# Optimization experiments

Measured on AMD Instinct MI355X. Metric: run time of the kernel, lower is better.

The kernel has to match this reference:

```python
import jax, jax.numpy as jnp
import numpy as np

W_L1, W_NORMAL, W_LAPLACIAN = 1.0, 1.0, 0.1
NORM_EPS = 1e-6   # F.normalize eps
COS_EPS = 1e-8    # F.cosine_similarity default eps


def setup_inputs() -> dict:
    key = jax.random.key(0)
    k1, k2, k3, k4, k5, k6 = jax.random.split(key, 6)
    N, F, NNZ = 1_000_000, 2_000_000, 8_000_000
    return {
        "V_rec": jax.random.normal(k1, (N, 3), dtype=jnp.float32),
        "V_gt": jax.random.normal(k2, (N, 3), dtype=jnp.float32),
        "faces": jax.random.randint(k3, (F, 3), 0, N, dtype=jnp.int64)
        if jax.config.jax_enable_x64 else jax.random.randint(k3, (F, 3), 0, N, dtype=jnp.int32),
        "L_rows": jax.random.randint(k4, (NNZ,), 0, N, dtype=jnp.int32),
        "L_cols": jax.random.randint(k5, (NNZ,), 0, N, dtype=jnp.int32),
        "L_vals": jax.random.normal(k6, (NNZ,), dtype=jnp.float32),
    }


def _vertex_normals(verts, faces):
    # gather verts by face indices: [F,3] each
    v0 = verts[faces[:, 0]]
    v1 = verts[faces[:, 1]]
    v2 = verts[faces[:, 2]]
    face_normals = jnp.cross(v1 - v0, v2 - v0)  # [F,3]
    vn = (jnp.zeros_like(verts)
          .at[faces[:, 0]].add(face_normals)
          .at[faces[:, 1]].add(face_normals)
          .at[faces[:, 2]].add(face_normals))
    norm = jnp.linalg.norm(vn, axis=1, keepdims=True)
    return vn / jnp.maximum(norm, NORM_EPS)


def _cosine_sim(a, b):
    dot = jnp.sum(a * b, axis=1)
    na = jnp.linalg.norm(a, axis=1)
    nb = jnp.linalg.norm(b, axis=1)
    return dot / (jnp.maximum(na, COS_EPS) * jnp.maximum(nb, COS_EPS))


def _spmm(rows, cols, vals, V):
    # sparse [N,N] @ dense [N,3] via gather + segment_sum
    return jax.ops.segment_sum(vals[:, None] * V[cols], rows, num_segments=V.shape[0])


def reference(V_rec, V_gt, faces, L_rows, L_cols, L_vals):
    # L1 term
    loss_l1 = jnp.mean(jnp.abs(V_rec - V_gt))
    # Normal cosine term
    normals_gt = _vertex_normals(V_gt, faces)
    normals_rec = _vertex_normals(V_rec, faces)
    cos_n = jnp.nan_to_num(_cosine_sim(normals_rec, normals_gt), nan=1.0)
    loss_normal = jnp.mean(1.0 - cos_n)
    # Laplacian cosine term
    delta_gt = _spmm(L_rows, L_cols, L_vals, V_gt)
    delta_rec = _spmm(L_rows, L_cols, L_vals, V_rec)
    cos_l = jnp.nan_to_num(_cosine_sim(delta_rec, delta_gt), nan=1.0)
    loss_laplacian = jnp.mean(1.0 - cos_l)
    finite = jnp.isfinite(delta_gt).all() & jnp.isfinite(delta_rec).all()
    loss_laplacian = jnp.where(finite, loss_laplacian, 0.0)
    return W_L1 * loss_l1 + W_NORMAL * loss_normal + W_LAPLACIAN * loss_laplacian
```

## Files before the change

### kernel.cpp

```cpp
#include <hip/hip_runtime.h>
#include <hip/hip_bf16.h>

#define NORM_EPS_F 1e-6f
#define COS_EPS_F  1e-8f
#define BK   512
#define BKSH 9
#define NBGMAX 2048
#define CHF1 2048
#define CHL1 4096
#define K2   32

__device__ __forceinline__ void atomAddF(float* p, float v) {
    unsafeAtomicAdd(p, v);
}

template<int NV>
__device__ __forceinline__ void blockReduceAtomicN(float (&v)[NV], float* dst) {
    #pragma unroll
    for (int off = 32; off > 0; off >>= 1) {
        #pragma unroll
        for (int k = 0; k < NV; ++k) v[k] += __shfl_down(v[k], off, 64);
    }
    __shared__ float red[4][NV];
    int wave = threadIdx.x >> 6, lane = threadIdx.x & 63;
    if (lane == 0) {
        #pragma unroll
        for (int k = 0; k < NV; ++k) red[wave][k] = v[k];
    }
    __syncthreads();
    if (threadIdx.x == 0) {
        float s[NV];
        #pragma unroll
        for (int k = 0; k < NV; ++k) s[k] = 0.f;
        for (int w = 0; w < 4; ++w)
            #pragma unroll
            for (int k = 0; k < NV; ++k) s[k] += red[w][k];
        #pragma unroll
        for (int k = 0; k < NV; ++k) atomAddF(&dst[k], s[k]);
    }
}


__global__ void __launch_bounds__(256) pack_l1_kernel(
    const float* __restrict__ Vr, const float* __restrict__ Vg,
    float4* __restrict__ Vp, float* __restrict__ accum, int N)
{
    int i = blockIdx.x * blockDim.x + threadIdx.x;
    float l1[1] = {0.f};
    if (i < N) {
        float rx = Vr[3 * i], ry = Vr[3 * i + 1], rz = Vr[3 * i + 2];
        float gx = Vg[3 * i], gy = Vg[3 * i + 1], gz = Vg[3 * i + 2];
        Vp[2 * i]     = make_float4(rx, ry, rz, 0.f);
        Vp[2 * i + 1] = make_float4(gx, gy, gz, 0.f);
        l1[0] = fabsf(rx - gx) + fabsf(ry - gy) + fabsf(rz - gz);
    }
    blockReduceAtomicN<1>(l1, &accum[0]);
}

__global__ void __launch_bounds__(256) fn_kernel(
    const float4* __restrict__ Vp, const int* __restrict__ faces,
    float4* __restrict__ FN, int F)
{
    int half = (F + 1) >> 1;
    int t = blockIdx.x * blockDim.x + threadIdx.x;
    if (t >= half) return;
    int fi[2] = {t, t + half};
    int n = (fi[1] < F) ? 2 : 1;
    int idx[2][3];
    #pragma unroll
    for (int k = 0; k < 2; ++k) if (k < n) {
        idx[k][0] = faces[3 * fi[k]];
        idx[k][1] = faces[3 * fi[k] + 1];
        idx[k][2] = faces[3 * fi[k] + 2];
    }
    float4 r0[2], r1[2], r2[2], g0[2], g1[2], g2[2];
    #pragma unroll
    for (int k = 0; k < 2; ++k) if (k < n) {
        r0[k] = Vp[2 * idx[k][0]]; g0[k] = Vp[2 * idx[k][0] + 1];
        r1[k] = Vp[2 * idx[k][1]]; g1[k] = Vp[2 * idx[k][1] + 1];
        r2[k] = Vp[2 * idx[k][2]]; g2[k] = Vp[2 * idx[k][2] + 1];
    }
    #pragma unroll
    for (int k = 0; k < 2; ++k) if (k < n) {
        float ax = r1[k].x - r0[k].x, ay = r1[k].y - r0[k].y, az = r1[k].z - r0[k].z;
        float bx = r2[k].x - r0[k].x, by = r2[k].y - r0[k].y, bz = r2[k].z - r0[k].z;
        FN[2 * fi[k]] = make_float4(ay * bz - az * by, az * bx - ax * bz, ax * by - ay * bx, 0.f);
        ax = g1[k].x - g0[k].x; ay = g1[k].y - g0[k].y; az = g1[k].z - g0[k].z;
        bx = g2[k].x - g0[k].x; by = g2[k].y - g0[k].y; bz = g2[k].z - g0[k].z;
        FN[2 * fi[k] + 1] = make_float4(ay * bz - az * by, az * bx - ax * bz, ax * by - ay * bx, 0.f);
    }
}


__global__ void __launch_bounds__(256) bucket_F1(
    const int* __restrict__ faces, int* __restrict__ cntC,
    unsigned* __restrict__ recA, unsigned char* __restrict__ recC,
    int capC, int F, int b0, int bcnt, int chunk)
{
    __shared__ int hist[64];
    int f0 = blockIdx.x * chunk, f1 = min(f0 + chunk, F);
    if (threadIdx.x < 64) hist[threadIdx.x] = 0;
    __syncthreads();
    for (int f = f0 + threadIdx.x; f < f1; f += 256) {
        #pragma unroll
        for (int c = 0; c < 3; ++c) {
            unsigned fb = ((unsigned)faces[3 * f + c] >> BKSH) - (unsigned)b0;
            if (fb < (unsigned)bcnt) atomicAdd(&hist[fb >> 5], 1);
        }
    }
    __syncthreads();
    if (threadIdx.x < 64) {
        int h = hist[threadIdx.x];
        if (h) hist[threadIdx.x] = atomicAdd(&cntC[threadIdx.x], h);
    }
    __syncthreads();
    for (int f = f0 + threadIdx.x; f < f1; f += 256) {
        #pragma unroll
        for (int c = 0; c < 3; ++c) {
            int v = faces[3 * f + c];
            unsigned fb = ((unsigned)v >> BKSH) - (unsigned)b0;
            if (fb < (unsigned)bcnt) {
                int pos = atomicAdd(&hist[fb >> 5], 1);
                if (pos < capC) {
                    size_t idx = (size_t)(fb >> 5) * capC + pos;
                    recA[idx] = ((unsigned)f << BKSH) | ((unsigned)v & (BK - 1));
                    recC[idx] = (unsigned char)(fb & 31);
                }
            }
        }
    }
}

__global__ void __launch_bounds__(256) bucket_L1(
    const int* __restrict__ rows, const int* __restrict__ cols,
    const float* __restrict__ vals, int* __restrict__ cntC,
    int2* __restrict__ recA, unsigned char* __restrict__ recC,
    int capC, int nnz, int b0, int bcnt, int chunk)
{
    __shared__ int hist[64];
    int i0 = blockIdx.x * chunk, i1 = min(i0 + chunk, nnz);
    if (threadIdx.x < 64) hist[threadIdx.x] = 0;
    __syncthreads();
    for (int i = i0 + threadIdx.x; i < i1; i += 256) {
        unsigned fb = ((unsigned)rows[i] >> BKSH) - (unsigned)b0;
        if (fb < (unsigned)bcnt) atomicAdd(&hist[fb >> 5], 1);
    }
    __syncthreads();
    if (threadIdx.x < 64) {
        int h = hist[threadIdx.x];
        if (h) hist[threadIdx.x] = atomicAdd(&cntC[threadIdx.x], h);
    }
    __syncthreads();
    for (int i = i0 + threadIdx.x; i < i1; i += 256) {
        int r = rows[i];
        unsigned fb = ((unsigned)r >> BKSH) - (unsigned)b0;
        if (fb < (unsigned)bcnt) {
            int pos = atomicAdd(&hist[fb >> 5], 1);
            if (pos < capC) {
                size_t idx = (size_t)(fb >> 5) * capC + pos;
                recA[idx] = make_int2(
                    (int)(((unsigned)cols[i] << BKSH) | ((unsigned)r & (BK - 1))),
                    __float_as_int(vals[i]));
                recC[idx] = (unsigned char)(fb & 31);
            }
        }
    }
}


__global__ void __launch_bounds__(256) bucket_F2(
    const int* __restrict__ cntC, const unsigned* __restrict__ recA,
    const unsigned char* __restrict__ recC, int capC,
    int* __restrict__ cntFine, unsigned* __restrict__ fine, int capF)
{
    __shared__ int hist[32];
    int c = blockIdx.x;
    int K = gridDim.y, k = blockIdx.y;
    int ch = (capC + K - 1) / K;
    int n = min(cntC[c], capC);
    int i0 = k * ch, i1 = min(i0 + ch, n);
    if (threadIdx.x < 32) hist[threadIdx.x] = 0;
    __syncthreads();
    const size_t base = (size_t)c * capC;
    for (int i = i0 + threadIdx.x; i < i1; i += 256)
        atomicAdd(&hist[recC[base + i]], 1);
    __syncthreads();
    if (threadIdx.x < 32) {
        int h = hist[threadIdx.x];
        if (h) hist[threadIdx.x] = atomicAdd(&cntFine[(c << 5) + threadIdx.x], h);
    }
    __syncthreads();
    for (int i = i0 + threadIdx.x; i < i1; i += 256) {
        int fic = recC[base + i];
        int pos = atomicAdd(&hist[fic], 1);
        if (pos < capF)
            fine[(size_t)((c << 5) + fic) * capF + pos] = recA[base + i];
    }
}

__global__ void __launch_bounds__(256) bucket_L2(
    const int* __restrict__ cntC, const int2* __restrict__ recA,
    const unsigned char* __restrict__ recC, int capC,
    int* __restrict__ cntFine, int2* __restrict__ fine, int capL)
{
    __shared__ int hist[32];
    int c = blockIdx.x;
    int K = gridDim.y, k = blockIdx.y;
    int ch = (capC + K - 1) / K;
    int n = min(cntC[c], capC);
    int i0 = k * ch, i1 = min(i0 + ch, n);
    if (threadIdx.x < 32) hist[threadIdx.x] = 0;
    __syncthreads();
    const size_t base = (size_t)c * capC;
    for (int i = i0 + threadIdx.x; i < i1; i += 256)
        atomicAdd(&hist[recC[base + i]], 1);
    __syncthreads();
    if (threadIdx.x < 32) {
        int h = hist[threadIdx.x];
        if (h) hist[threadIdx.x] = atomicAdd(&cntFine[(c << 5) + threadIdx.x], h);
    }
    __syncthreads();
    for (int i = i0 + threadIdx.x; i < i1; i += 256) {
        int fic = recC[base + i];
        int pos = atomicAdd(&hist[fic], 1);
        if (pos < capL)
            fine[(size_t)((c << 5) + fic) * capL + pos] = recA[base + i];
    }
}


__global__ void __launch_bounds__(256) accum_normals_kernel(
    const float4* __restrict__ Vp, const float4* __restrict__ FN,
    const int* __restrict__ faces,
    const int* __restrict__ cnt, const unsigned* __restrict__ recF, int capF,
    float* __restrict__ accum, int N, int b0, int use_fn)
{
    __shared__ float vnr[3 * BK];
    __shared__ float vng[3 * BK];
    int g = blockIdx.x;
    for (int i = threadIdx.x; i < 3 * BK; i += blockDim.x) { vnr[i] = 0.f; vng[i] = 0.f; }
    __syncthreads();

    const unsigned* rec = recF + (size_t)g * capF;
    int n = min(cnt[g], capF);
    int i = threadIdx.x;
    if (use_fn) {
        for (; i + 768 < n; i += 1024) {
            unsigned rc[4];
            rc[0] = rec[i]; rc[1] = rec[i + 256]; rc[2] = rec[i + 512]; rc[3] = rec[i + 768];
            float4 nr[4], ng[4];
            #pragma unroll
            for (int k = 0; k < 4; ++k) {
                int f = rc[k] >> BKSH;
                nr[k] = FN[2 * f];
                ng[k] = FN[2 * f + 1];
            }
            #pragma unroll
            for (int k = 0; k < 4; ++k) {
                int lv = rc[k] & (BK - 1);
                atomicAdd(&vnr[3 * lv + 0], nr[k].x);
                atomicAdd(&vnr[3 * lv + 1], nr[k].y);
                atomicAdd(&vnr[3 * lv + 2], nr[k].z);
                atomicAdd(&vng[3 * lv + 0], ng[k].x);
                atomicAdd(&vng[3 * lv + 1], ng[k].y);
                atomicAdd(&vng[3 * lv + 2], ng[k].z);
            }
        }
    }
    for (; i < n; i += 256) {
        unsigned rc = rec[i];
        int lv = rc & (BK - 1);
        int f  = rc >> BKSH;
        float4 nr, ng;
        if (use_fn) {
            nr = FN[2 * f];
            ng = FN[2 * f + 1];
        } else {
            int i0 = faces[3 * f], i1 = faces[3 * f + 1], i2 = faces[3 * f + 2];
            float4 r0 = Vp[2 * i0], r1 = Vp[2 * i1], r2 = Vp[2 * i2];
            float4 g0 = Vp[2 * i0 + 1], g1 = Vp[2 * i1 + 1], g2 = Vp[2 * i2 + 1];
            float ax = r1.x - r0.x, ay = r1.y - r0.y, az = r1.z - r0.z;
            float bx = r2.x - r0.x, by = r2.y - r0.y, bz = r2.z - r0.z;
            nr = make_float4(ay * bz - az * by, az * bx - ax * bz, ax * by - ay * bx, 0.f);
            ax = g1.x - g0.x; ay = g1.y - g0.y; az = g1.z - g0.z;
            bx = g2.x - g0.x; by = g2.y - g0.y; bz = g2.z - g0.z;
            ng = make_float4(ay * bz - az * by, az * bx - ax * bz, ax * by - ay * bx, 0.f);
        }
        atomicAdd(&vnr[3 * lv + 0], nr.x);
        atomicAdd(&vnr[3 * lv + 1], nr.y);
        atomicAdd(&vnr[3 * lv + 2], nr.z);
        atomicAdd(&vng[3 * lv + 0], ng.x);
        atomicAdd(&vng[3 * lv + 1], ng.y);
        atomicAdd(&vng[3 * lv + 2], ng.z);
    }
    __syncthreads();

    float ln[1] = {0.f};
    for (int lv = threadIdx.x; lv < BK; lv += blockDim.x) {
        int gv = ((b0 + g) << BKSH) + lv;
        if (gv < N) {
            float ax = vnr[3 * lv], ay = vnr[3 * lv + 1], az = vnr[3 * lv + 2];
            float bx = vng[3 * lv], by = vng[3 * lv + 1], bz = vng[3 * lv + 2];
            float na = sqrtf(ax * ax + ay * ay + az * az);
            float nb = sqrtf(bx * bx + by * by + bz * bz);
            float ia = 1.0f / fmaxf(na, NORM_EPS_F);
            float ib = 1.0f / fmaxf(nb, NORM_EPS_F);
            ax *= ia; ay *= ia; az *= ia;
            bx *= ib; by *= ib; bz *= ib;
            float dot = ax * bx + ay * by + az * bz;
            float nna = sqrtf(ax * ax + ay * ay + az * az);
            float nnb = sqrtf(bx * bx + by * by + bz * bz);
            float cosn = dot / (fmaxf(nna, COS_EPS_F) * fmaxf(nnb, COS_EPS_F));
            if (isnan(cosn)) cosn = 1.0f;
            ln[0] += 1.0f - cosn;
        }
    }
    blockReduceAtomicN<1>(ln, &accum[1]);
}

__global__ void __launch_bounds__(256) accum_lap_kernel(
    const float4* __restrict__ Vp,
    const int* __restrict__ cnt, const int2* __restrict__ recL, int capL,
    float* __restrict__ accum, int N, int b0)
{
    __shared__ float dlr[3 * BK];
    __shared__ float dlg[3 * BK];
    int g = blockIdx.x;
    for (int i = threadIdx.x; i < 3 * BK; i += blockDim.x) { dlr[i] = 0.f; dlg[i] = 0.f; }
    __syncthreads();

    const int2* rec = recL + (size_t)g * capL;
    int n = min(cnt[g], capL);
    int i = threadIdx.x;
    for (; i + 768 < n; i += 1024) {
        int2 rc[4];
        rc[0] = rec[i]; rc[1] = rec[i + 256]; rc[2] = rec[i + 512]; rc[3] = rec[i + 768];
        float4 pr[4], pg[4];
        #pragma unroll
        for (int k = 0; k < 4; ++k) {
            int col = (unsigned)rc[k].x >> BKSH;
            pr[k] = Vp[2 * col];
            pg[k] = Vp[2 * col + 1];
        }
        #pragma unroll
        for (int k = 0; k < 4; ++k) {
            int lv = (unsigned)rc[k].x & (BK - 1);
            float v = __int_as_float(rc[k].y);
            atomicAdd(&dlr[3 * lv + 0], v * pr[k].x);
            atomicAdd(&dlr[3 * lv + 1], v * pr[k].y);
            atomicAdd(&dlr[3 * lv + 2], v * pr[k].z);
            atomicAdd(&dlg[3 * lv + 0], v * pg[k].x);
            atomicAdd(&dlg[3 * lv + 1], v * pg[k].y);
            atomicAdd(&dlg[3 * lv + 2], v * pg[k].z);
        }
    }
    for (; i < n; i += 256) {
        int2 rc = rec[i];
        unsigned u = (unsigned)rc.x;
        int lv  = u & (BK - 1);
        int col = u >> BKSH;
        float v = __int_as_float(rc.y);
        float4 pr = Vp[2 * col];
        float4 pg = Vp[2 * col + 1];
        atomicAdd(&dlr[3 * lv + 0], v * pr.x);
        atomicAdd(&dlr[3 * lv + 1], v * pr.y);
        atomicAdd(&dlr[3 * lv + 2], v * pr.z);
        atomicAdd(&dlg[3 * lv + 0], v * pg.x);
        atomicAdd(&dlg[3 * lv + 1], v * pg.y);
        atomicAdd(&dlg[3 * lv + 2], v * pg.z);
    }
    __syncthreads();

    float vals2[2] = {0.f, 0.f};
    for (int lv = threadIdx.x; lv < BK; lv += blockDim.x) {
        int gv = ((b0 + g) << BKSH) + lv;
        if (gv < N) {
            float px = dlr[3 * lv], py = dlr[3 * lv + 1], pz = dlr[3 * lv + 2];
            float qx = dlg[3 * lv], qy = dlg[3 * lv + 1], qz = dlg[3 * lv + 2];
            bool fin = isfinite(px) && isfinite(py) && isfinite(pz) &&
                       isfinite(qx) && isfinite(qy) && isfinite(qz);
            vals2[1] += fin ? 0.f : 1.f;
            float dotl = px * qx + py * qy + pz * qz;
            float npn = sqrtf(px * px + py * py + pz * pz);
            float nqn = sqrtf(qx * qx + qy * qy + qz * qz);
            float cosl = dotl / (fmaxf(npn, COS_EPS_F) * fmaxf(nqn, COS_EPS_F));
            if (isnan(cosl)) cosl = 1.0f;
            vals2[0] += 1.0f - cosl;
        }
    }
    blockReduceAtomicN<2>(vals2, &accum[2]);
}

__global__ void finalize_kernel(const float* __restrict__ accum,
                                float* __restrict__ out, int N)
{
    float invN = 1.0f / (float)N;
    float l1 = accum[0] * invN * (1.0f / 3.0f);
    float ln = accum[1] * invN;
    float ll = (accum[3] > 0.0f) ? 0.0f : accum[2] * invN;
    out[0] = 1.0f * l1 + 1.0f * ln + 0.1f * ll;
}


__global__ void __launch_bounds__(256) face_normals_kernel(
    const float* __restrict__ Vr, const float* __restrict__ Vg,
    const int* __restrict__ faces,
    float* __restrict__ vn_rec, float* __restrict__ vn_gt, int F)
{
    int f = blockIdx.x * blockDim.x + threadIdx.x;
    if (f >= F) return;
    int i0 = faces[3 * f + 0], i1 = faces[3 * f + 1], i2 = faces[3 * f + 2];
    {
        float v0x = Vr[3 * i0], v0y = Vr[3 * i0 + 1], v0z = Vr[3 * i0 + 2];
        float v1x = Vr[3 * i1], v1y = Vr[3 * i1 + 1], v1z = Vr[3 * i1 + 2];
        float v2x = Vr[3 * i2], v2y = Vr[3 * i2 + 1], v2z = Vr[3 * i2 + 2];
        float ax = v1x - v0x, ay = v1y - v0y, az = v1z - v0z;
        float bx = v2x - v0x, by = v2y - v0y, bz = v2z - v0z;
        float nx = ay * bz - az * by, ny = az * bx - ax * bz, nz = ax * by - ay * bx;
        atomAddF(&vn_rec[3 * i0], nx); atomAddF(&vn_rec[3 * i0 + 1], ny); atomAddF(&vn_rec[3 * i0 + 2], nz);
        atomAddF(&vn_rec[3 * i1], nx); atomAddF(&vn_rec[3 * i1 + 1], ny); atomAddF(&vn_rec[3 * i1 + 2], nz);
        atomAddF(&vn_rec[3 * i2], nx); atomAddF(&vn_rec[3 * i2 + 1], ny); atomAddF(&vn_rec[3 * i2 + 2], nz);
    }
    {
        float v0x = Vg[3 * i0], v0y = Vg[3 * i0 + 1], v0z = Vg[3 * i0 + 2];
        float v1x = Vg[3 * i1], v1y = Vg[3 * i1 + 1], v1z = Vg[3 * i1 + 2];
        float v2x = Vg[3 * i2], v2y = Vg[3 * i2 + 1], v2z = Vg[3 * i2 + 2];
        float ax = v1x - v0x, ay = v1y - v0y, az = v1z - v0z;
        float bx = v2x - v0x, by = v2y - v0y, bz = v2z - v0z;
        float nx = ay * bz - az * by, ny = az * bx - ax * bz, nz = ax * by - ay * bx;
        atomAddF(&vn_gt[3 * i0], nx); atomAddF(&vn_gt[3 * i0 + 1], ny); atomAddF(&vn_gt[3 * i0 + 2], nz);
        atomAddF(&vn_gt[3 * i1], nx); atomAddF(&vn_gt[3 * i1 + 1], ny); atomAddF(&vn_gt[3 * i1 + 2], nz);
        atomAddF(&vn_gt[3 * i2], nx); atomAddF(&vn_gt[3 * i2 + 1], ny); atomAddF(&vn_gt[3 * i2 + 2], nz);
    }
}

__global__ void __launch_bounds__(256) spmm_kernel(
    const float* __restrict__ Vr, const float* __restrict__ Vg,
    const int* __restrict__ rows, const int* __restrict__ cols,
    const float* __restrict__ vals,
    float* __restrict__ dl_rec, float* __restrict__ dl_gt, int nnz)
{
    int i = blockIdx.x * blockDim.x + threadIdx.x;
    if (i >= nnz) return;
    int r = rows[i], c = cols[i];
    float v = vals[i];
    atomAddF(&dl_rec[3 * r], v * Vr[3 * c]);
    atomAddF(&dl_rec[3 * r + 1], v * Vr[3 * c + 1]);
    atomAddF(&dl_rec[3 * r + 2], v * Vr[3 * c + 2]);
    atomAddF(&dl_gt[3 * r], v * Vg[3 * c]);
    atomAddF(&dl_gt[3 * r + 1], v * Vg[3 * c + 1]);
    atomAddF(&dl_gt[3 * r + 2], v * Vg[3 * c + 2]);
}

__global__ void __launch_bounds__(256) reduce_kernel(
    const float* __restrict__ Vr, const float* __restrict__ Vg,
    const float* __restrict__ vn_rec, const float* __restrict__ vn_gt,
    const float* __restrict__ dl_rec, const float* __restrict__ dl_gt,
    float* __restrict__ accum, int N)
{
    int i = blockIdx.x * blockDim.x + threadIdx.x;
    float l1 = 0.0f, ln = 0.0f, ll = 0.0f, nonfin = 0.0f;
    if (i < N) {
        float rx = Vr[3 * i], ry = Vr[3 * i + 1], rz = Vr[3 * i + 2];
        float gx = Vg[3 * i], gy = Vg[3 * i + 1], gz = Vg[3 * i + 2];
        l1 = fabsf(rx - gx) + fabsf(ry - gy) + fabsf(rz - gz);
        float ax = vn_rec[3 * i], ay = vn_rec[3 * i + 1], az = vn_rec[3 * i + 2];
        float bx = vn_gt[3 * i],  by = vn_gt[3 * i + 1],  bz = vn_gt[3 * i + 2];
        float na = sqrtf(ax * ax + ay * ay + az * az);
        float nb = sqrtf(bx * bx + by * by + bz * bz);
        float ia = 1.0f / fmaxf(na, NORM_EPS_F);
        float ib = 1.0f / fmaxf(nb, NORM_EPS_F);
        ax *= ia; ay *= ia; az *= ia; bx *= ib; by *= ib; bz *= ib;
        float dot = ax * bx + ay * by + az * bz;
        float nna = sqrtf(ax * ax + ay * ay + az * az);
        float nnb = sqrtf(bx * bx + by * by + bz * bz);
        float cosn = dot / (fmaxf(nna, COS_EPS_F) * fmaxf(nnb, COS_EPS_F));
        if (isnan(cosn)) cosn = 1.0f;
        ln = 1.0f - cosn;
        float px = dl_rec[3 * i], py = dl_rec[3 * i + 1], pz = dl_rec[3 * i + 2];
        float qx = dl_gt[3 * i],  qy = dl_gt[3 * i + 1],  qz = dl_gt[3 * i + 2];
        bool fin = isfinite(px) && isfinite(py) && isfinite(pz) &&
                   isfinite(qx) && isfinite(qy) && isfinite(qz);
        nonfin = fin ? 0.0f : 1.0f;
        float dotl = px * qx + py * qy + pz * qz;
        float npn = sqrtf(px * px + py * py + pz * pz);
        float nqn = sqrtf(qx * qx + qy * qy + qz * qz);
        float cosl = dotl / (fmaxf(npn, COS_EPS_F) * fmaxf(nqn, COS_EPS_F));
        if (isnan(cosl)) cosl = 1.0f;
        ll = 1.0f - cosl;
    }
    float a[1] = {l1};  blockReduceAtomicN<1>(a, &accum[0]);
    float b[1] = {ln};  blockReduceAtomicN<1>(b, &accum[1]);
    float c2[2] = {ll, nonfin}; blockReduceAtomicN<2>(c2, &accum[2]);
}


extern "C" void kernel_launch(void* const* d_in, const int* in_sizes, int n_in,
                              void* d_out, int out_size, void* d_ws, size_t ws_size,
                              hipStream_t stream)
{
    const float* Vr    = (const float*)d_in[0];
    const float* Vg    = (const float*)d_in[1];
    const int*   faces = (const int*)d_in[2];
    const int*   Lr    = (const int*)d_in[3];
    const int*   Lc    = (const int*)d_in[4];
    const float* Lv    = (const float*)d_in[5];

    const int N   = in_sizes[0] / 3;
    const int F   = in_sizes[2] / 3;
    const int NNZ = in_sizes[3];
    const int NB  = (N + BK - 1) >> BKSH;

    float* ws = (float*)d_ws;
    const int B = 256;

    const long long totW   = (long long)(ws_size / 4);
    const long long fixedW = 4 + 64 + NBGMAX;
    const long long vpW    = 8LL * N;
    const long long arenaW = totW - fixedW - vpW;
    const long long fnW    = 8LL * F;

    const int capF = 3 * F / (NB > 0 ? NB : 1) + 1 + 640;
    const int capL = NNZ / (NB > 0 ? NB : 1) + 1 + 640;

    auto fwords = [&](int nbg) -> long long {
        long long nc = (nbg + 31) / 32, capC = 32LL * capF;
        return nc * capC + (nc * capC + 3) / 4 + (long long)nbg * capF + 4;
    };
    auto lwords = [&](int nbg) -> long long {
        long long nc = (nbg + 31) / 32, capC = 32LL * capL;
        return nc * capC * 2 + (((nc * capC + 3) / 4 + 1) & ~1LL) + (long long)nbg * capL * 2 + 4;
    };

    int NBG_F = NB < NBGMAX ? NB : NBGMAX;
    bool tierA = (arenaW - fnW) >= fwords(64);
    long long arenaF = tierA ? (arenaW - fnW) : arenaW;
    while (NBG_F > 64 && fwords(NBG_F) > arenaF) NBG_F -= 32;
    int NBG_L = NB < NBGMAX ? NB : NBGMAX;
    while (NBG_L > 64 && lwords(NBG_L) > arenaW) NBG_L -= 32;

    bool fast = (N <= (1 << 20)) && (F <= (1 << 22)) &&
                NBG_F >= 64 && NBG_L >= 64 &&
                fwords(NBG_F) <= arenaF && lwords(NBG_L) <= arenaW &&
                arenaW > 0;

    if (fast) {
        float*  accum   = ws;
        int*    cntC    = (int*)(ws + 4);
        int*    cntFine = (int*)(ws + 68);
        float4* Vp      = (float4*)(ws + fixedW);
        float*  arena   = ws + fixedW + vpW;

        const long long NCF = (NBG_F + 31) / 32, capCF = 32LL * capF;
        float4*        FN    = (float4*)arena;
        float*         fbase = tierA ? (arena + fnW) : arena;
        unsigned*      recAF = (unsigned*)fbase;
        unsigned char* recCF = (unsigned char*)(recAF + NCF * capCF);
        unsigned*      fineF = (unsigned*)(fbase + NCF * capCF + (NCF * capCF + 3) / 4);

        const long long NCL = (NBG_L + 31) / 32, capCL = 32LL * capL;
        int2*          recAL = (int2*)arena;
        unsigned char* recCL = (unsigned char*)(recAL + NCL * capCL);
        const long long bytesWL = ((NCL * capCL + 3) / 4 + 1) & ~1LL;
        int2*          fineL = (int2*)(arena + NCL * capCL * 2 + bytesWL);

        hipMemsetAsync(accum, 0, 4 * sizeof(float), stream);

        pack_l1_kernel<<<dim3((N + B - 1) / B), dim3(B), 0, stream>>>(Vr, Vg, Vp, accum, N);
        if (tierA) {
            int half = (F + 1) >> 1;
            fn_kernel<<<dim3((half + B - 1) / B), dim3(B), 0, stream>>>(Vp, faces, FN, F);
        }

        int passF = (NB + NBG_F - 1) / NBG_F;
        for (int p = 0; p < passF; ++p) {
            int b0 = p * NBG_F;
            int bcnt = NB - b0 < NBG_F ? NB - b0 : NBG_F;
            int nc = (bcnt + 31) / 32;
            hipMemsetAsync(ws + 4, 0, (64 + NBGMAX) * sizeof(int), stream);
            bucket_F1<<<dim3((F + CHF1 - 1) / CHF1), dim3(B), 0, stream>>>(
                faces, cntC, recAF, recCF, (int)capCF, F, b0, bcnt, CHF1);
            bucket_F2<<<dim3(nc, K2), dim3(B), 0, stream>>>(
                cntC, recAF, recCF, (int)capCF, cntFine, fineF, capF);
            accum_normals_kernel<<<dim3(bcnt), dim3(B), 0, stream>>>(
                Vp, FN, faces, cntFine, fineF, capF, accum, N, b0, tierA ? 1 : 0);
        }

        int passL = (NB + NBG_L - 1) / NBG_L;
        for (int p = 0; p < passL; ++p) {
            int b0 = p * NBG_L;
            int bcnt = NB - b0 < NBG_L ? NB - b0 : NBG_L;
            int nc = (bcnt + 31) / 32;
            hipMemsetAsync(ws + 4, 0, (64 + NBGMAX) * sizeof(int), stream);
            bucket_L1<<<dim3((NNZ + CHL1 - 1) / CHL1), dim3(B), 0, stream>>>(
                Lr, Lc, Lv, cntC, recAL, recCL, (int)capCL, NNZ, b0, bcnt, CHL1);
            bucket_L2<<<dim3(nc, K2), dim3(B), 0, stream>>>(
                cntC, recAL, recCL, (int)capCL, cntFine, fineL, capL);
            accum_lap_kernel<<<dim3(bcnt), dim3(B), 0, stream>>>(
                Vp, cntFine, fineL, capL, accum, N, b0);
        }
        finalize_kernel<<<dim3(1), dim3(1), 0, stream>>>(accum, (float*)d_out, N);
    } else {
        float* vn_rec = ws;
        float* vn_gt  = ws + (size_t)3 * N;
        float* dl_rec = ws + (size_t)6 * N;
        float* dl_gt  = ws + (size_t)9 * N;
        float* accum  = ws + (size_t)12 * N;
        hipMemsetAsync(d_ws, 0, ((size_t)12 * N + 4) * sizeof(float), stream);
        face_normals_kernel<<<dim3((F + B - 1) / B), dim3(B), 0, stream>>>(Vr, Vg, faces, vn_rec, vn_gt, F);
        spmm_kernel<<<dim3((NNZ + B - 1) / B), dim3(B), 0, stream>>>(Vr, Vg, Lr, Lc, Lv, dl_rec, dl_gt, NNZ);
        reduce_kernel<<<dim3((N + B - 1) / B), dim3(B), 0, stream>>>(Vr, Vg, vn_rec, vn_gt, dl_rec, dl_gt, accum, N);
        finalize_kernel<<<dim3(1), dim3(1), 0, stream>>>(accum, (float*)d_out, N);
    }
}
```

Baseline: 1.098 ms.

## Sub-bucket Laplacian records by column octant to localize vertex gathers

Bucket_L1 now encodes the high bits of the column index (an octant of the vertex range) into the per-record byte, and bucket_L2 splits each row bucket into 8 column-octant sub-buckets. The accumulate kernel walks the octants in order, so the vertex gathers of concurrently running blocks fall within a narrower address range and should hit cache more often. The cost is more fine-bucket counters, a larger 256-entry histogram, per-sub-bucket capacity padding that can overflow under skew, and a shallower unroll in the inner loop.

```diff
diff --git a/kernel.cpp b/kernel.cpp
--- a/kernel.cpp
+++ b/kernel.cpp
@@ -9,6 +9,7 @@
 #define CHF1 2048
 #define CHL1 4096
 #define K2   32
+#define NOCT 8
 
 __device__ __forceinline__ void atomAddF(float* p, float v) {
     unsafeAtomicAdd(p, v);
@@ -135,7 +136,7 @@
     const int* __restrict__ rows, const int* __restrict__ cols,
     const float* __restrict__ vals, int* __restrict__ cntC,
     int2* __restrict__ recA, unsigned char* __restrict__ recC,
-    int capC, int nnz, int b0, int bcnt, int chunk)
+    int capC, int nnz, int b0, int bcnt, int chunk, int octsh)
 {
     __shared__ int hist[64];
     int i0 = blockIdx.x * chunk, i1 = min(i0 + chunk, nnz);
@@ -158,10 +159,11 @@
             int pos = atomicAdd(&hist[fb >> 5], 1);
             if (pos < capC) {
                 size_t idx = (size_t)(fb >> 5) * capC + pos;
+                unsigned c = (unsigned)cols[i];
                 recA[idx] = make_int2(
-                    (int)(((unsigned)cols[i] << BKSH) | ((unsigned)r & (BK - 1))),
+                    (int)((c << BKSH) | ((unsigned)r & (BK - 1))),
                     __float_as_int(vals[i]));
-                recC[idx] = (unsigned char)(fb & 31);
+                recC[idx] = (unsigned char)(((fb & 31) << 3) | (c >> octsh));
             }
         }
     }
@@ -201,30 +203,30 @@
 __global__ void __launch_bounds__(256) bucket_L2(
     const int* __restrict__ cntC, const int2* __restrict__ recA,
     const unsigned char* __restrict__ recC, int capC,
-    int* __restrict__ cntFine, int2* __restrict__ fine, int capL)
-{
-    __shared__ int hist[32];
+    int* __restrict__ cntFine, int2* __restrict__ fine, int capS)
+{
+    __shared__ int hist[256];
     int c = blockIdx.x;
     int K = gridDim.y, k = blockIdx.y;
     int ch = (capC + K - 1) / K;
     int n = min(cntC[c], capC);
     int i0 = k * ch, i1 = min(i0 + ch, n);
-    if (threadIdx.x < 32) hist[threadIdx.x] = 0;
+    hist[threadIdx.x] = 0;
     __syncthreads();
     const size_t base = (size_t)c * capC;
     for (int i = i0 + threadIdx.x; i < i1; i += 256)
         atomicAdd(&hist[recC[base + i]], 1);
     __syncthreads();
-    if (threadIdx.x < 32) {
+    {
         int h = hist[threadIdx.x];
-        if (h) hist[threadIdx.x] = atomicAdd(&cntFine[(c << 5) + threadIdx.x], h);
+        if (h) hist[threadIdx.x] = atomicAdd(&cntFine[(c << 8) + threadIdx.x], h);
     }
     __syncthreads();
     for (int i = i0 + threadIdx.x; i < i1; i += 256) {
         int fic = recC[base + i];
         int pos = atomicAdd(&hist[fic], 1);
-        if (pos < capL)
-            fine[(size_t)((c << 5) + fic) * capL + pos] = recA[base + i];
+        if (pos < capS)
+            fine[(size_t)((c << 8) + fic) * capS + pos] = recA[base + i];
     }
 }
 
@@ -320,7 +322,7 @@
 
 __global__ void __launch_bounds__(256) accum_lap_kernel(
     const float4* __restrict__ Vp,
-    const int* __restrict__ cnt, const int2* __restrict__ recL, int capL,
+    const int* __restrict__ cntFine, const int2* __restrict__ recL, int capS,
     float* __restrict__ accum, int N, int b0)
 {
     __shared__ float dlr[3 * BK];
@@ -329,45 +331,45 @@
     for (int i = threadIdx.x; i < 3 * BK; i += blockDim.x) { dlr[i] = 0.f; dlg[i] = 0.f; }
     __syncthreads();
 
-    const int2* rec = recL + (size_t)g * capL;
-    int n = min(cnt[g], capL);
-    int i = threadIdx.x;
-    for (; i + 768 < n; i += 1024) {
-        int2 rc[4];
-        rc[0] = rec[i]; rc[1] = rec[i + 256]; rc[2] = rec[i + 512]; rc[3] = rec[i + 768];
-        float4 pr[4], pg[4];
-        #pragma unroll
-        for (int k = 0; k < 4; ++k) {
-            int col = (unsigned)rc[k].x >> BKSH;
-            pr[k] = Vp[2 * col];
-            pg[k] = Vp[2 * col + 1];
-        }
-        #pragma unroll
-        for (int k = 0; k < 4; ++k) {
-            int lv = (unsigned)rc[k].x & (BK - 1);
-            float v = __int_as_float(rc[k].y);
-            atomicAdd(&dlr[3 * lv + 0], v * pr[k].x);
-            atomicAdd(&dlr[3 * lv + 1], v * pr[k].y);
-            atomicAdd(&dlr[3 * lv + 2], v * pr[k].z);
-            atomicAdd(&dlg[3 * lv + 0], v * pg[k].x);
-            atomicAdd(&dlg[3 * lv + 1], v * pg[k].y);
-            atomicAdd(&dlg[3 * lv + 2], v * pg[k].z);
-        }
-    }
-    for (; i < n; i += 256) {
-        int2 rc = rec[i];
-        unsigned u = (unsigned)rc.x;
-        int lv  = u & (BK - 1);
-        int col = u >> BKSH;
-        float v = __int_as_float(rc.y);
-        float4 pr = Vp[2 * col];
-        float4 pg = Vp[2 * col + 1];
-        atomicAdd(&dlr[3 * lv + 0], v * pr.x);
-        atomicAdd(&dlr[3 * lv + 1], v * pr.y);
-        atomicAdd(&dlr[3 * lv + 2], v * pr.z);
-        atomicAdd(&dlg[3 * lv + 0], v * pg.x);
-        atomicAdd(&dlg[3 * lv + 1], v * pg.y);
-        atomicAdd(&dlg[3 * lv + 2], v * pg.z);
+    for (int oct = 0; oct < NOCT; ++oct) {
+        const int2* rec = recL + ((size_t)g * NOCT + oct) * capS;
+        int n = min(cntFine[g * NOCT + oct], capS);
+        int i = threadIdx.x;
+        for (; i + 256 < n; i += 512) {
+            int2 rc0 = rec[i], rc1 = rec[i + 256];
+            int c0 = (unsigned)rc0.x >> BKSH, c1 = (unsigned)rc1.x >> BKSH;
+            float4 pr0 = Vp[2 * c0], pg0 = Vp[2 * c0 + 1];
+            float4 pr1 = Vp[2 * c1], pg1 = Vp[2 * c1 + 1];
+            int lv0 = (unsigned)rc0.x & (BK - 1), lv1 = (unsigned)rc1.x & (BK - 1);
+            float v0 = __int_as_float(rc0.y), v1 = __int_as_float(rc1.y);
+            atomicAdd(&dlr[3 * lv0 + 0], v0 * pr0.x);
+            atomicAdd(&dlr[3 * lv0 + 1], v0 * pr0.y);
+            atomicAdd(&dlr[3 * lv0 + 2], v0 * pr0.z);
+            atomicAdd(&dlg[3 * lv0 + 0], v0 * pg0.x);
+            atomicAdd(&dlg[3 * lv0 + 1], v0 * pg0.y);
+            atomicAdd(&dlg[3 * lv0 + 2], v0 * pg0.z);
+            atomicAdd(&dlr[3 * lv1 + 0], v1 * pr1.x);
+            atomicAdd(&dlr[3 * lv1 + 1], v1 * pr1.y);
+            atomicAdd(&dlr[3 * lv1 + 2], v1 * pr1.z);
+            atomicAdd(&dlg[3 * lv1 + 0], v1 * pg1.x);
+            atomicAdd(&dlg[3 * lv1 + 1], v1 * pg1.y);
+            atomicAdd(&dlg[3 * lv1 + 2], v1 * pg1.z);
+        }
+        for (; i < n; i += 256) {
+            int2 rc = rec[i];
+            unsigned u = (unsigned)rc.x;
+            int lv  = u & (BK - 1);
+            int col = u >> BKSH;
+            float v = __int_as_float(rc.y);
+            float4 pr = Vp[2 * col];
+            float4 pg = Vp[2 * col + 1];
+            atomicAdd(&dlr[3 * lv + 0], v * pr.x);
+            atomicAdd(&dlr[3 * lv + 1], v * pr.y);
+            atomicAdd(&dlr[3 * lv + 2], v * pr.z);
+            atomicAdd(&dlg[3 * lv + 0], v * pg.x);
+            atomicAdd(&dlg[3 * lv + 1], v * pg.y);
+            atomicAdd(&dlg[3 * lv + 2], v * pg.z);
+        }
     }
     __syncthreads();
 
@@ -514,14 +516,19 @@
     float* ws = (float*)d_ws;
     const int B = 256;
 
+    int lg = 0;
+    while ((1LL << lg) < N) ++lg;
+    const int octsh = lg > 3 ? lg - 3 : 0;
+
     const long long totW   = (long long)(ws_size / 4);
-    const long long fixedW = 4 + 64 + NBGMAX;
+    const long long fixedW = 4 + 64 + (long long)NBGMAX * NOCT;
     const long long vpW    = 8LL * N;
     const long long arenaW = totW - fixedW - vpW;
     const long long fnW    = 8LL * F;
 
     const int capF = 3 * F / (NB > 0 ? NB : 1) + 1 + 640;
     const int capL = NNZ / (NB > 0 ? NB : 1) + 1 + 640;
+    const int capS = NNZ / ((NB > 0 ? NB : 1) * NOCT) + 1 + 256;
 
     auto fwords = [&](int nbg) -> long long {
         long long nc = (nbg + 31) / 32, capC = 32LL * capF;
@@ -529,7 +536,8 @@
     };
     auto lwords = [&](int nbg) -> long long {
         long long nc = (nbg + 31) / 32, capC = 32LL * capL;
-        return nc * capC * 2 + (((nc * capC + 3) / 4 + 1) & ~1LL) + (long long)nbg * capL * 2 + 4;
+        return nc * capC * 2 + (((nc * capC + 3) / 4 + 1) & ~1LL)
+             + (long long)nbg * NOCT * capS * 2 + 4;
     };
 
     int NBG_F = NB < NBGMAX ? NB : NBGMAX;
@@ -577,7 +585,7 @@
             int b0 = p * NBG_F;
             int bcnt = NB - b0 < NBG_F ? NB - b0 : NBG_F;
             int nc = (bcnt + 31) / 32;
-            hipMemsetAsync(ws + 4, 0, (64 + NBGMAX) * sizeof(int), stream);
+            hipMemsetAsync(ws + 4, 0, (64 + (size_t)NBGMAX) * sizeof(int), stream);
             bucket_F1<<<dim3((F + CHF1 - 1) / CHF1), dim3(B), 0, stream>>>(
                 faces, cntC, recAF, recCF, (int)capCF, F, b0, bcnt, CHF1);
             bucket_F2<<<dim3(nc, K2), dim3(B), 0, stream>>>(
@@ -591,13 +599,13 @@
             int b0 = p * NBG_L;
             int bcnt = NB - b0 < NBG_L ? NB - b0 : NBG_L;
             int nc = (bcnt + 31) / 32;
-            hipMemsetAsync(ws + 4, 0, (64 + NBGMAX) * sizeof(int), stream);
+            hipMemsetAsync(ws + 4, 0, (64 + (size_t)NBGMAX * NOCT) * sizeof(int), stream);
             bucket_L1<<<dim3((NNZ + CHL1 - 1) / CHL1), dim3(B), 0, stream>>>(
-                Lr, Lc, Lv, cntC, recAL, recCL, (int)capCL, NNZ, b0, bcnt, CHL1);
+                Lr, Lc, Lv, cntC, recAL, recCL, (int)capCL, NNZ, b0, bcnt, CHL1, octsh);
             bucket_L2<<<dim3(nc, K2), dim3(B), 0, stream>>>(
-                cntC, recAL, recCL, (int)capCL, cntFine, fineL, capL);
+                cntC, recAL, recCL, (int)capCL, cntFine, fineL, capS);
             accum_lap_kernel<<<dim3(bcnt), dim3(B), 0, stream>>>(
-                Vp, cntFine, fineL, capL, accum, N, b0);
+                Vp, cntFine, fineL, capS, accum, N, b0);
         }
         finalize_kernel<<<dim3(1), dim3(1), 0, stream>>>(accum, (float*)d_out, N);
     } else {
```

After: 1.144 ms. 1.04x slower.
